# Kernel tuning notes

Measured on AMD Instinct MI355X. Metric: run time of the kernel, lower is better.

Reference implementation:

```python
import jax, jax.numpy as jnp
import numpy as np

DOWN_RATIO = 4.0
K_DET = 300          # max detections kept per image (YOLOv5 default)
P_PTS = 128          # contour points per instance (deep-snake)
CONF_THR = 0.2
IOU_THR = 0.3
MAX_WH = 4096.0      # class offset for class-aware NMS
DILATIONS = (1, 1, 1, 2, 2, 4, 4)
N_ITER = 2           # snake evolution iterations


def cir_conv(x, w, b, dil):
    # circular 1D conv along point dim; x [N,C,P], w [O,C,K]
    k = w.shape[-1]
    pad = dil * (k - 1) // 2
    xp = jnp.concatenate([x[..., x.shape[-1] - pad:], x, x[..., :pad]], axis=-1)
    y = jax.lax.conv_general_dilated(xp, w, window_strides=(1,), padding='VALID',
                                     rhs_dilation=(dil,),
                                     dimension_numbers=('NCH', 'OIH', 'NCH'))
    return y + b[None, :, None]


def snake_offsets(z, w_head, b_head, w_res, b_res, w_fuse, b_fuse, w_p1, b_p1, w_p2, b_p2):
    # z [N,66,P] -> offsets [N,2,P]
    states = [z]
    x = jax.nn.relu(cir_conv(z, w_head, b_head, 1))
    states.append(x)
    for i, d in enumerate(DILATIONS):
        x = jax.nn.relu(cir_conv(x, w_res[i], b_res[i], d)) + x
        states.append(x)
    state = jnp.concatenate(states, axis=1)            # [N,1090,P]
    fused = jax.nn.relu(cir_conv(state, w_fuse, b_fuse, 1))  # [N,256,P]
    h = jax.nn.relu(cir_conv(fused, w_p1, b_p1, 1))
    return cir_conv(h, w_p2, b_p2, 1)                  # [N,2,P]


def bilinear_sample(feat, pts):
    # feat [C,H,W]; pts [K,P,2] (x,y) in feature pixels -> [K,C,P]
    C, H, W = feat.shape
    x = jnp.clip(pts[..., 0], 0.0, W - 1.0)
    y = jnp.clip(pts[..., 1], 0.0, H - 1.0)
    x0f = jnp.clip(jnp.floor(x), 0.0, W - 2.0)
    y0f = jnp.clip(jnp.floor(y), 0.0, H - 2.0)
    x0 = x0f.astype(jnp.int32); y0 = y0f.astype(jnp.int32)
    dx = x - x0f; dy = y - y0f
    f = feat.reshape(C, H * W)
    def g(ix, iy):
        return f[:, iy * W + ix]                       # [C,K,P]
    out = (g(x0, y0) * (1 - dx) * (1 - dy) + g(x0 + 1, y0) * dx * (1 - dy)
           + g(x0, y0 + 1) * (1 - dx) * dy + g(x0 + 1, y0 + 1) * dx * dy)
    return out.transpose(1, 0, 2)


def nms_single(boxes, scores, cls):
    # boxes [K,4] xyxy sorted desc by score; class-aware greedy NMS -> keep mask [K]
    K = boxes.shape[0]
    b = boxes + cls[:, None] * MAX_WH
    area = (b[:, 2] - b[:, 0]) * (b[:, 3] - b[:, 1])
    lt = jnp.maximum(b[:, None, :2], b[None, :, :2])
    rb = jnp.minimum(b[:, None, 2:], b[None, :, 2:])
    wh = jnp.clip(rb - lt, 0.0)
    inter = wh[..., 0] * wh[..., 1]
    iou = inter / (area[:, None] + area[None, :] - inter + 1e-9)
    def body(i, keep):
        sup = (iou[i] > IOU_THR) & (jnp.arange(K) > i) & keep[i]
        return keep & (~sup)
    return jax.lax.fori_loop(0, K, body, jnp.ones((K,), bool))


def reference(pred, feat, conv_w, conv_b, w_head, b_head, w_res, b_res,
              w_fuse, b_fuse, w_p1, b_p1, w_p2, b_p2):
    B, N, D = pred.shape
    # ---- non_max_suppression(pred, 0.2, 0.3) ----
    score_all = pred[..., 4:5] * pred[..., 5:]          # obj * cls
    score = score_all.max(-1)                           # [B,N]
    cls = jnp.argmax(score_all, -1)                     # [B,N]
    s_masked = jnp.where(score > CONF_THR, score, 0.0)
    top_s, top_i = jax.lax.top_k(s_masked, K_DET)       # [B,K]
    xywh = jnp.take_along_axis(pred[..., :4], top_i[..., None], axis=1)
    boxes = jnp.concatenate([xywh[..., :2] - xywh[..., 2:] / 2,
                             xywh[..., :2] + xywh[..., 2:] / 2], axis=-1)
    cls_k = jnp.take_along_axis(cls, top_i, axis=1).astype(jnp.float32)
    keep = jax.vmap(nms_single)(boxes, top_s, cls_k)
    valid = keep & (top_s > CONF_THR)                   # [B,K]
    detection = jnp.concatenate([boxes, top_s[..., None], cls_k[..., None]], -1)
    boxes_ds = boxes / DOWN_RATIO                       # feature-scale boxes
    ct = jnp.stack([(boxes_ds[..., 0] + boxes_ds[..., 2]) / 2,
                    (boxes_ds[..., 1] + boxes_ds[..., 3]) / 2], -1)  # [B,K,2]
    Bf, C, H, W = feat.shape
    up = jax.image.resize(feat, (Bf, C, 2 * H, 2 * W), method='linear')
    cf = jax.lax.conv_general_dilated(up, conv_w, (1, 1), 'SAME',
                                      dimension_numbers=('NCHW', 'OIHW', 'NCHW'))
    cf = jax.nn.silu(cf + conv_b[None, :, None, None])  # [B,64,160,160]
    # ---- snake contour evolution ----
    half = jnp.maximum((boxes_ds[..., 2:] - boxes_ds[..., :2]) / 2, 1e-3)  # [B,K,2]
    theta = jnp.arange(P_PTS, dtype=jnp.float32) * (2 * np.pi / P_PTS)
    ring = jnp.stack([jnp.cos(theta), jnp.sin(theta)], -1)                 # [P,2]
    pts = ct[:, :, None, :] + half[:, :, None, :] * ring[None, None]       # [B,K,P,2]
    for _ in range(N_ITER):
        fpts = jax.vmap(bilinear_sample)(cf, pts)                          # [B,K,64,P]
        rel = ((pts - ct[:, :, None, :]) / half[:, :, None, :]).transpose(0, 1, 3, 2)
        z = jnp.concatenate([fpts, rel], axis=2)                           # [B,K,66,P]
        z = z.reshape(B * K_DET, 66, P_PTS)
        off = snake_offsets(z, w_head, b_head, w_res, b_res, w_fuse, b_fuse,
                            w_p1, b_p1, w_p2, b_p2)
        pts = pts + off.reshape(B, K_DET, 2, P_PTS).transpose(0, 1, 3, 2)
    pts = pts * valid[..., None, None].astype(pts.dtype)
    return detection, ct, pts, valid


def setup_inputs():
    key = jax.random.key(0)
    ks = jax.random.split(key, 16)
    B, N, NC = 16, 25200, 80
    cx = jax.random.uniform(ks[0], (B, N, 1)) * 640.0
    cy = jax.random.uniform(ks[1], (B, N, 1)) * 640.0
    w = jax.random.uniform(ks[2], (B, N, 1)) * 120.0 + 8.0
    h = jax.random.uniform(ks[3], (B, N, 1)) * 120.0 + 8.0
    conf = jax.random.uniform(ks[4], (B, N, 1 + NC))
    pred = jnp.concatenate([cx, cy, w, h, conf], -1)
    feat = jax.random.normal(ks[5], (B, 128, 80, 80))
    p = lambda k, s: jax.random.normal(k, s) * 0.05
    return {
        'pred': pred, 'feat': feat,
        'conv_w': p(ks[6], (64, 128, 3, 3)), 'conv_b': jnp.zeros((64,)),
        'w_head': p(ks[7], (128, 66, 9)), 'b_head': jnp.zeros((128,)),
        'w_res': p(ks[8], (7, 128, 128, 9)), 'b_res': jnp.zeros((7, 128)),
        'w_fuse': p(ks[9], (256, 1090, 1)), 'b_fuse': jnp.zeros((256,)),
        'w_p1': p(ks[10], (64, 256, 1)), 'b_p1': jnp.zeros((64,)),
        'w_p2': p(ks[11], (2, 64, 1)), 'b_p2': jnp.zeros((2,)),
    }
```

## Files before the change

kernel.cpp:

```cpp
#include <hip/hip_runtime.h>
#include <hip/hip_bf16.h>
#include <math.h>

typedef unsigned int u32;
typedef unsigned long long u64;
typedef unsigned short u16;

#define NB 16
#define NPRED 25200
#define ND 85
#define NCLS 80
#define KDET 300
#define PPTS 128
#define NINST (NB*KDET)
#define CONF_T 0.2f
#define IOU_T 0.3f
#define MAX_WH_ 4096.0f
#define NBKT 8192

#define CH 1120
#define STROW 143360

typedef __attribute__((ext_vector_type(8))) short bhalf8;
typedef __attribute__((ext_vector_type(4))) float f32x4;

__device__ __forceinline__ float b2f(u16 u){ return __uint_as_float((u32)u << 16); }
__device__ __forceinline__ u16 f2b(float v){ __hip_bfloat16 h = __float2bfloat16(v); return *(u16*)&h; }

__global__ __launch_bounds__(256) void k_score(const float* __restrict__ pred,
        float* __restrict__ score, int* __restrict__ cls){
  int i = blockIdx.x*256 + threadIdx.x;
  if (i >= NB*NPRED) return;
  const float* r = pred + (size_t)i*ND;
  float obj = r[4];
  float best = obj*r[5]; int bc = 0;
  for (int c = 1; c < NCLS; ++c){
    float v = obj*r[5+c];
    if (v > best){ best = v; bc = c; }
  }
  score[i] = (best > CONF_T) ? best : 0.f;
  cls[i] = bc;
}

__global__ __launch_bounds__(1024) void k_topk(const float* __restrict__ score,
        int* __restrict__ top_i, float* __restrict__ top_s){
  __shared__ int hist[NBKT];
  __shared__ int part[1024];
  __shared__ u64 keys[1024];
  __shared__ int s_bstar, s_cnt;
  int b = blockIdx.x, t = threadIdx.x;
  const float* s = score + (size_t)b*NPRED;
  for (int i = t; i < NBKT; i += 1024) hist[i] = 0;
  __syncthreads();
  for (int i = t; i < NPRED; i += 1024){
    float v = s[i];
    if (v > 0.f){
      int bk = (int)(v * (float)NBKT); if (bk > NBKT-1) bk = NBKT-1;
      atomicAdd(&hist[bk], 1);
    }
  }
  __syncthreads();
  int psum = 0;
  for (int j = 0; j < 8; ++j) psum += hist[t*8+j];
  part[t] = psum;
  __syncthreads();
  if (t == 0){
    int cum = 0, bstar = 0;
    for (int q = 1023; q >= 0; --q){
      if (cum + part[q] >= KDET){
        int c2 = cum; int bb;
        for (bb = q*8+7; bb >= q*8; --bb){
          c2 += hist[bb];
          if (c2 >= KDET) break;
        }
        if (bb < q*8) bb = q*8;
        bstar = bb;
        break;
      }
      cum += part[q];
    }
    s_bstar = bstar;
    s_cnt = 0;
  }
  keys[t] = 0ull;
  __syncthreads();
  int bstar = s_bstar;
  for (int i = t; i < NPRED; i += 1024){
    float v = s[i];
    if (v > 0.f){
      int bk = (int)(v * (float)NBKT); if (bk > NBKT-1) bk = NBKT-1;
      if (bk >= bstar){
        int pos = atomicAdd(&s_cnt, 1);
        if (pos < 1024){
          keys[pos] = ((u64)__float_as_uint(v) << 32) | (u32)(~(u32)i);
        }
      }
    }
  }
  __syncthreads();
  for (int k = 2; k <= 1024; k <<= 1){
    for (int j = k>>1; j > 0; j >>= 1){
      int ixj = t ^ j;
      if (ixj > t){
        u64 a = keys[t], c = keys[ixj];
        bool up = ((t & k) == 0);
        bool sw = up ? (a < c) : (a > c);
        if (sw){ keys[t] = c; keys[ixj] = a; }
      }
      __syncthreads();
    }
  }
  if (t < KDET){
    u64 key = keys[t];
    float v; int idx;
    if (key == 0ull){ v = 0.f; idx = 0; }
    else { v = __uint_as_float((u32)(key >> 32)); idx = (int)(~(u32)(key & 0xffffffffull)); }
    top_s[b*KDET + t] = v;
    top_i[b*KDET + t] = idx;
  }
}

__global__ __launch_bounds__(384) void k_nms(const float* __restrict__ pred,
        const int* __restrict__ top_i, const float* __restrict__ top_s,
        const int* __restrict__ clsb,
        float* __restrict__ det_out, float* __restrict__ ct_out, float* __restrict__ pts_out,
        float* __restrict__ ct_ws, float* __restrict__ half_ws, int* __restrict__ valid_ws){
  __shared__ float bx0[KDET], bx1[KDET], bx2[KDET], bx3[KDET], ar[KDET];
  __shared__ float rx0[KDET], rx1[KDET], rx2[KDET], rx3[KDET];
  __shared__ float sc[KDET], cl[KDET];
  __shared__ float ctxs[KDET], ctys[KDET], hxs[KDET], hys[KDET];
  __shared__ int keep[KDET];
  int b = blockIdx.x, t = threadIdx.x;
  for (int i = t; i < KDET; i += 384){
    int idx = top_i[b*KDET + i];
    const float* r = pred + ((size_t)b*NPRED + idx)*ND;
    float cx = r[0], cy = r[1], w = r[2], h = r[3];
    float x1 = cx - w/2.f, y1 = cy - h/2.f, x2 = cx + w/2.f, y2 = cy + h/2.f;
    float c = (float)clsb[(size_t)b*NPRED + idx];
    float o = c * MAX_WH_;
    float a0 = x1 + o, a1 = y1 + o, a2 = x2 + o, a3 = y2 + o;
    bx0[i]=a0; bx1[i]=a1; bx2[i]=a2; bx3[i]=a3;
    ar[i] = (a2-a0)*(a3-a1);
    rx0[i]=x1; rx1[i]=y1; rx2[i]=x2; rx3[i]=y2;
    sc[i] = top_s[b*KDET + i];
    cl[i] = c;
    keep[i] = 1;
  }
  __syncthreads();
  for (int i = 0; i < KDET; ++i){
    if (keep[i]){
      float b0=bx0[i], b1=bx1[i], b2=bx2[i], b3=bx3[i], ai=ar[i];
      for (int j = i+1+t; j < KDET; j += 384){
        float ltx = fmaxf(b0, bx0[j]);
        float lty = fmaxf(b1, bx1[j]);
        float rbx = fminf(b2, bx2[j]);
        float rby = fminf(b3, bx3[j]);
        float ww = rbx - ltx; ww = ww > 0.f ? ww : 0.f;
        float hh = rby - lty; hh = hh > 0.f ? hh : 0.f;
        float inter = ww*hh;
        float iou = inter / (ai + ar[j] - inter + 1e-9f);
        if (iou > IOU_T) keep[j] = 0;
      }
    }
    __syncthreads();
  }
  for (int i = t; i < KDET; i += 384){
    int v = (keep[i] && (sc[i] > CONF_T)) ? 1 : 0;
    valid_ws[b*KDET + i] = v;
    size_t o6 = ((size_t)b*KDET + i)*6;
    det_out[o6+0]=rx0[i]; det_out[o6+1]=rx1[i]; det_out[o6+2]=rx2[i]; det_out[o6+3]=rx3[i];
    det_out[o6+4]=sc[i];  det_out[o6+5]=cl[i];
    float bd0 = rx0[i]/4.f, bd1 = rx1[i]/4.f, bd2 = rx2[i]/4.f, bd3 = rx3[i]/4.f;
    float cx = (bd0+bd2)/2.f, cy = (bd1+bd3)/2.f;
    float hx = (bd2-bd0)/2.f; hx = hx > 1e-3f ? hx : 1e-3f;
    float hy = (bd3-bd1)/2.f; hy = hy > 1e-3f ? hy : 1e-3f;
    ct_out[((size_t)b*KDET+i)*2+0] = cx;
    ct_out[((size_t)b*KDET+i)*2+1] = cy;
    ct_ws[((size_t)b*KDET+i)*2+0] = cx;
    ct_ws[((size_t)b*KDET+i)*2+1] = cy;
    half_ws[((size_t)b*KDET+i)*2+0] = hx;
    half_ws[((size_t)b*KDET+i)*2+1] = hy;
    ctxs[i]=cx; ctys[i]=cy; hxs[i]=hx; hys[i]=hy;
  }
  __syncthreads();
  for (int e = t; e < KDET*PPTS; e += 384){
    int i = e >> 7, p = e & 127;
    float th = (float)p * 0.04908738521234052f;
    size_t o = ((size_t)(b*KDET + i)*PPTS + p)*2;
    pts_out[o+0] = ctxs[i] + hxs[i]*cosf(th);
    pts_out[o+1] = ctys[i] + hys[i]*sinf(th);
  }
}

__global__ __launch_bounds__(256) void k_cnn(const float* __restrict__ feat,
        const float* __restrict__ cw, const float* __restrict__ cb,
        __hip_bfloat16* __restrict__ cf){
  __shared__ float up[324];
  __shared__ float wl[576];
  int b = blockIdx.x;
  int tile = blockIdx.y;
  int ty0 = (tile/10)*16, tx0 = (tile - (tile/10)*10)*16;
  int t = threadIdx.x;
  int py = t >> 4, px = t & 15;
  int oy = ty0 + py, ox = tx0 + px;
  float acc[64];
  #pragma unroll
  for (int o = 0; o < 64; ++o) acc[o] = 0.f;
  for (int ic = 0; ic < 128; ++ic){
    __syncthreads();
    const float* fin = feat + ((size_t)b*128 + ic)*6400;
    for (int u = t; u < 324; u += 256){
      int r = u/18;
      int uy = ty0 - 1 + r, ux = tx0 - 1 + (u - r*18);
      float val = 0.f;
      if (uy >= 0 && uy < 160 && ux >= 0 && ux < 160){
        float cyf = 0.5f*(float)uy - 0.25f;
        float cxf = 0.5f*(float)ux - 0.25f;
        float fy0 = floorf(cyf), fx0 = floorf(cxf);
        float fy = cyf - fy0, fx = cxf - fx0;
        int y0 = (int)fy0, x0 = (int)fx0;
        int y0c = y0 < 0 ? 0 : (y0 > 79 ? 79 : y0);
        int y1c = y0+1 > 79 ? 79 : (y0+1 < 0 ? 0 : y0+1);
        int x0c = x0 < 0 ? 0 : (x0 > 79 ? 79 : x0);
        int x1c = x0+1 > 79 ? 79 : (x0+1 < 0 ? 0 : x0+1);
        float v00 = fin[y0c*80+x0c], v01 = fin[y0c*80+x1c];
        float v10 = fin[y1c*80+x0c], v11 = fin[y1c*80+x1c];
        val = v00*(1.f-fy)*(1.f-fx) + v01*(1.f-fy)*fx + v10*fy*(1.f-fx) + v11*fy*fx;
      }
      up[u] = val;
    }
    for (int u = t; u < 576; u += 256){
      int o = u/9;
      wl[u] = cw[((size_t)o*128 + ic)*9 + (u - o*9)];
    }
    __syncthreads();
    float v[9];
    #pragma unroll
    for (int k = 0; k < 9; ++k)
      v[k] = up[(py + k/3)*18 + (px + k%3)];
    #pragma unroll
    for (int o = 0; o < 64; ++o){
      float a = acc[o];
      #pragma unroll
      for (int k = 0; k < 9; ++k) a += wl[o*9+k]*v[k];
      acc[o] = a;
    }
  }
  size_t base = ((size_t)b*64)*25600 + (size_t)oy*160 + ox;
  #pragma unroll
  for (int o = 0; o < 64; ++o){
    float x = acc[o] + cb[o];
    float sg = 1.f / (1.f + __expf(-x));
    cf[base + (size_t)o*25600] = __float2bfloat16(x*sg);
  }
}

__global__ __launch_bounds__(256) void k_sample(const __hip_bfloat16* __restrict__ cf,
        const float* __restrict__ pts, const float* __restrict__ ct_ws,
        const float* __restrict__ half_ws, __hip_bfloat16* __restrict__ states,
        int base, int cnt){
  int e = blockIdx.x*256 + threadIdx.x;
  if (e >= cnt*PPTS) return;
  int li = e >> 7, p = e & 127;
  int g = base + li;
  int b = g / KDET;
  size_t po = ((size_t)g*PPTS + p)*2;
  float px = pts[po], py = pts[po+1];
  float ctx = ct_ws[g*2], cty = ct_ws[g*2+1];
  float hx = half_ws[g*2], hy = half_ws[g*2+1];
  __align__(16) u16 zl[66];
  zl[64] = f2b((px - ctx)/hx);
  zl[65] = f2b((py - cty)/hy);
  float x = px < 0.f ? 0.f : (px > 159.f ? 159.f : px);
  float y = py < 0.f ? 0.f : (py > 159.f ? 159.f : py);
  float x0f = floorf(x); x0f = x0f < 0.f ? 0.f : (x0f > 158.f ? 158.f : x0f);
  float y0f = floorf(y); y0f = y0f < 0.f ? 0.f : (y0f > 158.f ? 158.f : y0f);
  float dx = x - x0f, dy = y - y0f;
  int x0 = (int)x0f, y0 = (int)y0f;
  float w00 = (1.f-dx)*(1.f-dy), w01 = dx*(1.f-dy), w10 = (1.f-dx)*dy, w11 = dx*dy;
  const __hip_bfloat16* f = cf + (size_t)b*64*25600 + (size_t)y0*160 + x0;
  for (int c = 0; c < 64; ++c){
    const __hip_bfloat16* fc = f + (size_t)c*25600;
    float v00 = __bfloat162float(fc[0]);
    float v01 = __bfloat162float(fc[1]);
    float v10 = __bfloat162float(fc[160]);
    float v11 = __bfloat162float(fc[161]);
    zl[c] = f2b(v00*w00 + v01*w01 + v10*w10 + v11*w11);
  }
  u16* dst = (u16*)states + ((size_t)li*128 + p)*CH + 1024;
  #pragma unroll
  for (int w2 = 0; w2 < 64; w2 += 8) *(uint4*)(dst + w2) = *(const uint4*)(zl + w2);
  *(u32*)(dst + 64) = *(const u32*)(zl + 64);
}


template<int NSUB>
__device__ __forceinline__ void g_load_a(bhalf8* dst, const u16* Xb, int s, int dil,
                                         int rg0, int r16, int hi){
  int k = s / NSUB;
  int icb = (s - k*NSUB)*64 + hi*16;
  int shift = (k - 4)*dil;
  #pragma unroll
  for (int g = 0; g < 4; ++g){
    int row = (rg0 + g*16 + r16 + shift + 128) & 127;
    dst[g] = *(const bhalf8*)((const char*)Xb + row*256 + (icb ^ ((row & 7) << 4)));
  }
}
__device__ __forceinline__ void g_load_b(bhalf8* dst, const bhalf8* wf, int s, int lane, int sstride){
  const bhalf8* w = wf + (size_t)s*sstride + lane;
  #pragma unroll
  for (int ct = 0; ct < 8; ++ct) dst[ct] = w[ct*64];
}

#define MFMA_SET(A_, B_) { \
  _Pragma("unroll") \
  for (int g_ = 0; g_ < 4; ++g_){ \
    _Pragma("unroll") \
    for (int ct_ = 0; ct_ < 8; ++ct_) \
      acc[g_][ct_] = __builtin_amdgcn_mfma_f32_16x16x32_bf16((A_)[g_], (B_)[ct_], acc[g_][ct_], 0, 0, 0); \
  } }

template<int NSUB>
__device__ __forceinline__ void gemm_run(const u16* Xb, const bhalf8* wf, int s0, int s1,
    int dil, int rg0, int r16, int hi, int lane, f32x4 acc[4][8], int sstride){
  bhalf8 aA[4], bA[8], aB[4], bB[8];
  g_load_a<NSUB>(aA, Xb, s0, dil, rg0, r16, hi);
  g_load_b(bA, wf, s0, lane, sstride);
  int s = s0;
  for (; s + 1 < s1; s += 2){
    g_load_a<NSUB>(aB, Xb, s+1, dil, rg0, r16, hi);
    g_load_b(bB, wf, s+1, lane, sstride);
    MFMA_SET(aA, bA);
    if (s + 2 < s1){
      g_load_a<NSUB>(aA, Xb, s+2, dil, rg0, r16, hi);
      g_load_b(bA, wf, s+2, lane, sstride);
    }
    MFMA_SET(aB, bB);
  }
  if (s < s1) MFMA_SET(aA, bA);
}

__device__ __forceinline__ void epilogue(f32x4 acc[4][8], u16* Y, const u16* Xc,
    const float* __restrict__ bias, u16* gout, int gstride, int rg0, int r16, int hi){
  #pragma unroll
  for (int g = 0; g < 4; ++g){
    #pragma unroll
    for (int ct = 0; ct < 8; ++ct){
      int oc = ct*16 + r16;
      float bv = bias[oc];
      #pragma unroll
      for (int rr = 0; rr < 4; ++rr){
        int p = rg0 + g*16 + hi*4 + rr;
        float v = acc[g][ct][rr] + bv;
        v = v > 0.f ? v : 0.f;
        int lidx = (p*256 + ((oc*2) ^ ((p & 7) << 4))) >> 1;
        if (Xc) v += b2f(Xc[lidx]);
        u16 hu = f2b(v);
        if (Y) Y[lidx] = hu;
        gout[(size_t)p*gstride + oc] = hu;
      }
    }
  }
}

__global__ __launch_bounds__(128) void k_mega(__hip_bfloat16* __restrict__ states_,
    const u16* __restrict__ wfh, const float* __restrict__ bh,
    const u16* __restrict__ wfr, const float* __restrict__ brs){
  __shared__ u16 X[2][16384];
  int t = threadIdx.x, lane = t & 63, wid = t >> 6;
  int r16 = lane & 15, hi = lane >> 4;
  int rg0 = wid*64;
  u16* st = (u16*)states_ + (size_t)blockIdx.x*STROW;
  const bhalf8* WH = (const bhalf8*)wfh;
  const bhalf8* WR = (const bhalf8*)wfr;
  f32x4 acc[4][8];

  for (int i = t; i < 2048; i += 128){
    int p = i >> 4, c = i & 15;
    if (c < 12){
      uint4 v = *(const uint4*)(st + (size_t)p*CH + 1024 + c*8);
      *(uint4*)((char*)X[0] + p*256 + ((c*16) ^ ((p & 7) << 4))) = v;
    }
  }
  __syncthreads();

  #pragma unroll
  for (int g = 0; g < 4; ++g)
    #pragma unroll
    for (int ct = 0; ct < 8; ++ct) acc[g][ct] = (f32x4){0.f,0.f,0.f,0.f};
  gemm_run<3>(X[0], WH, 0, 27, 1, rg0, r16, hi, lane, acc, 512);
  epilogue(acc, X[1], nullptr, bh, st, CH, rg0, r16, hi);
  __syncthreads();

  int cur = 1;
  #pragma unroll 1
  for (int l = 0; l < 7; ++l){
    int dil = (l < 3) ? 1 : ((l < 5) ? 2 : 4);
    #pragma unroll
    for (int g = 0; g < 4; ++g)
      #pragma unroll
      for (int ct = 0; ct < 8; ++ct) acc[g][ct] = (f32x4){0.f,0.f,0.f,0.f};
    gemm_run<4>(X[cur], WR + (size_t)l*18432, 0, 36, dil, rg0, r16, hi, lane, acc, 512);
    epilogue(acc, X[cur^1], X[cur], brs + l*128, st + 128*(l+1), CH, rg0, r16, hi);
    __syncthreads();
    cur ^= 1;
  }
}

__global__ __launch_bounds__(256) void k_fuse(const __hip_bfloat16* __restrict__ states_,
    __hip_bfloat16* __restrict__ fusedb, const u16* __restrict__ wff,
    const float* __restrict__ bfu){
  __shared__ u16 XF[2][16384];
  int t = threadIdx.x, lane = t & 63, wid = t >> 6;
  int r16 = lane & 15, hi = lane >> 4;
  int wr = wid & 1, wc = wid >> 1;
  int rg0 = wr*64;
  const u16* st = (const u16*)states_ + (size_t)blockIdx.x*STROW;
  const bhalf8* WFp = (const bhalf8*)wff + wc*512;
  f32x4 acc[4][8];
  #pragma unroll
  for (int g = 0; g < 4; ++g)
    #pragma unroll
    for (int ct = 0; ct < 8; ++ct) acc[g][ct] = (f32x4){0.f,0.f,0.f,0.f};
  #pragma unroll 1
  for (int cc = 0; cc < 9; ++cc){
    __syncthreads();
    int ch0 = cc*128, nc = (cc == 8) ? 12 : 16;
    for (int i = t; i < 2048; i += 256){
      int p = i >> 4, c = i & 15;
      if (c < nc){
        uint4 v = *(const uint4*)(st + (size_t)p*CH + ch0 + c*8);
        *(uint4*)((char*)XF[cc & 1] + p*256 + ((c*16) ^ ((p & 7) << 4))) = v;
      }
    }
    __syncthreads();
    int s0 = cc*4, s1 = (cc == 8) ? 35 : (s0 + 4);
    gemm_run<4>(XF[cc & 1], WFp, s0, s1, 0, rg0, r16, hi, lane, acc, 1024);
  }
  u16* fo = (u16*)fusedb + (size_t)blockIdx.x*32768 + wc*128;
  epilogue(acc, nullptr, nullptr, bfu + wc*128, fo, 256, rg0, r16, hi);
}

__global__ __launch_bounds__(128) void k_p1p2(const __hip_bfloat16* __restrict__ fusedbuf,
        const float* __restrict__ wp1r, const float* __restrict__ bp1,
        const float* __restrict__ wp2, const float* __restrict__ bp2,
        float* __restrict__ pts, int base){
  int inst = blockIdx.x, p = threadIdx.x;
  const u16* f = (const u16*)fusedbuf + (size_t)inst*32768 + (size_t)p*256;
  float h[64];
  #pragma unroll
  for (int o = 0; o < 64; ++o) h[o] = bp1[o];
  for (int c8 = 0; c8 < 32; ++c8){
    uint4 v = *(const uint4*)(f + c8*8);
    const u16* vv = (const u16*)&v;
    #pragma unroll
    for (int j = 0; j < 8; ++j){
      float x = b2f(vv[j]);
      const float* w = wp1r + (size_t)(c8*8 + j)*64;
      #pragma unroll
      for (int o = 0; o < 64; ++o) h[o] += w[o]*x;
    }
  }
  float ox = bp2[0], oy = bp2[1];
  #pragma unroll
  for (int o = 0; o < 64; ++o){
    float hv = h[o] > 0.f ? h[o] : 0.f;
    ox += wp2[o]*hv;
    oy += wp2[64+o]*hv;
  }
  int g = base + inst;
  size_t po = ((size_t)g*PPTS + p)*2;
  pts[po]   += ox;
  pts[po+1] += oy;
}

__global__ __launch_bounds__(256) void k_final(float* __restrict__ pts,
        const int* __restrict__ valid_ws, float* __restrict__ valid_out){
  int e = blockIdx.x*256 + threadIdx.x;
  if (e < NINST) valid_out[e] = valid_ws[e] ? 1.f : 0.f;
  if (e < NINST*PPTS){
    float m = valid_ws[e >> 7] ? 1.f : 0.f;
    pts[(size_t)e*2]   *= m;
    pts[(size_t)e*2+1] *= m;
  }
}

__global__ __launch_bounds__(256) void k_pack_head(const float* __restrict__ w, u16* __restrict__ out){
  int e = blockIdx.x*256 + threadIdx.x;
  if (e >= 110592) return;
  int j = e & 7, l = (e >> 3) & 63, ct = (e >> 9) & 7, s = e >> 12;
  int oc = ct*16 + (l & 15);
  int k = s/3, icq = s - k*3;
  int ic = icq*32 + (l >> 4)*8 + j;
  float v = (ic < 66) ? w[(oc*66 + ic)*9 + k] : 0.f;
  out[e] = f2b(v);
}
__global__ __launch_bounds__(256) void k_pack_res(const float* __restrict__ w, u16* __restrict__ out){
  int e = blockIdx.x*256 + threadIdx.x;
  if (e >= 1032192) return;
  int lay = e / 147456, r = e - lay*147456;
  int j = r & 7, l = (r >> 3) & 63, ct = (r >> 9) & 7, s = r >> 12;
  int oc = ct*16 + (l & 15);
  int k = s >> 2;
  int ic = (s & 3)*32 + (l >> 4)*8 + j;
  out[e] = f2b(w[((size_t)(lay*128 + oc)*128 + ic)*9 + k]);
}
__global__ __launch_bounds__(256) void k_pack_fuse(const float* __restrict__ w, u16* __restrict__ out){
  int e = blockIdx.x*256 + threadIdx.x;
  if (e >= 286720) return;
  int j = e & 7, l = (e >> 3) & 63, ct = (e >> 9) & 15, s = e >> 13;
  int oc = ct*16 + (l & 15);
  int ch = s*32 + (l >> 4)*8 + j;
  float v = 0.f;
  if (ch < 1024) v = w[(size_t)oc*1090 + 66 + ch];
  else if (ch < 1090) v = w[(size_t)oc*1090 + (ch - 1024)];
  out[e] = f2b(v);
}
__global__ __launch_bounds__(256) void k_repack_p1(const float* __restrict__ w, float* __restrict__ wr){
  int e = blockIdx.x*256 + threadIdx.x;
  if (e >= 64*256) return;
  int oc = e / 256, ic = e - oc*256;
  wr[ic*64 + oc] = w[e];
}

extern "C" void kernel_launch(void* const* d_in, const int* in_sizes, int n_in,
                              void* d_out, int out_size, void* d_ws, size_t ws_size,
                              hipStream_t stream){
  (void)in_sizes; (void)n_in; (void)out_size;
  const float* pred   = (const float*)d_in[0];
  const float* feat   = (const float*)d_in[1];
  const float* conv_w = (const float*)d_in[2];
  const float* conv_b = (const float*)d_in[3];
  const float* w_head = (const float*)d_in[4];
  const float* b_head = (const float*)d_in[5];
  const float* w_res  = (const float*)d_in[6];
  const float* b_res  = (const float*)d_in[7];
  const float* w_fuse = (const float*)d_in[8];
  const float* b_fuse = (const float*)d_in[9];
  const float* w_p1   = (const float*)d_in[10];
  const float* b_p1   = (const float*)d_in[11];
  const float* w_p2   = (const float*)d_in[12];
  const float* b_p2   = (const float*)d_in[13];

  float* out = (float*)d_out;
  float* det_out   = out;
  float* ct_out    = out + 28800;
  float* pts_out   = out + 38400;
  float* valid_out = out + 1267200;

  char* wsb = (char*)d_ws;
  size_t woff = 0;
  auto walloc = [&](size_t bytes)->char*{
    char* p = wsb + woff;
    woff += (bytes + 255) & ~(size_t)255;
    return p;
  };
  __hip_bfloat16* cf = (__hip_bfloat16*)walloc((size_t)16*64*160*160*2);
  float* score   = (float*)walloc((size_t)NB*NPRED*4);
  int*   clsb    = (int*)  walloc((size_t)NB*NPRED*4);
  int*   top_i   = (int*)  walloc((size_t)NINST*4);
  float* top_s   = (float*)walloc((size_t)NINST*4);
  float* ct_ws   = (float*)walloc((size_t)NINST*2*4);
  float* half_ws = (float*)walloc((size_t)NINST*2*4);
  int*   valid_ws= (int*)  walloc((size_t)NINST*4);
  u16*   wfh     = (u16*)  walloc((size_t)110592*2);
  u16*   wfr     = (u16*)  walloc((size_t)1032192*2);
  u16*   wff     = (u16*)  walloc((size_t)286720*2);
  float* wr_p1   = (float*)walloc((size_t)16384*4);

  size_t per_inst = (size_t)STROW*2 + (size_t)32768*2;
  long long avail = (long long)ws_size - (long long)woff;
  int C = (int)(avail / (long long)per_inst);
  if (C > NINST) C = NINST;
  if (C < 1) C = 1;
  __hip_bfloat16* states   = (__hip_bfloat16*)walloc((size_t)C*STROW*2);
  __hip_bfloat16* fusedbuf = (__hip_bfloat16*)walloc((size_t)C*32768*2);

  k_pack_head<<<(110592+255)/256, 256, 0, stream>>>(w_head, wfh);
  k_pack_res <<<(1032192+255)/256, 256, 0, stream>>>(w_res, wfr);
  k_pack_fuse<<<(286720+255)/256, 256, 0, stream>>>(w_fuse, wff);
  k_repack_p1<<<(16384+255)/256, 256, 0, stream>>>(w_p1, wr_p1);

  k_score<<<(NB*NPRED+255)/256, 256, 0, stream>>>(pred, score, clsb);
  k_topk <<<NB, 1024, 0, stream>>>(score, top_i, top_s);
  k_nms  <<<NB, 384, 0, stream>>>(pred, top_i, top_s, clsb, det_out, ct_out, pts_out,
                                  ct_ws, half_ws, valid_ws);
  k_cnn  <<<dim3(16,100), 256, 0, stream>>>(feat, conv_w, conv_b, cf);

  for (int it = 0; it < 2; ++it){
    for (int base = 0; base < NINST; base += C){
      int cnt = NINST - base; if (cnt > C) cnt = C;
      k_sample<<<(cnt*PPTS+255)/256, 256, 0, stream>>>(cf, pts_out, ct_ws, half_ws, states, base, cnt);
      k_mega<<<cnt, 128, 0, stream>>>(states, wfh, b_head, wfr, b_res);
      k_fuse<<<cnt, 256, 0, stream>>>(states, fusedbuf, wff, b_fuse);
      k_p1p2<<<cnt, 128, 0, stream>>>(fusedbuf, wr_p1, b_p1, w_p2, b_p2, pts_out, base);
    }
  }
  k_final<<<(NINST*PPTS+255)/256, 256, 0, stream>>>(pts_out, valid_ws, valid_out);
}
```

Before: 10.87 ms.

## Fuse snake pipeline into one persistent kernel and retile the upsample conv

Sampling, head and residual convs, fuse conv, p1 and p2 now run in a single persistent kernel. Each block loops over instances for both snake iterations, replacing the per-chunk sequence of four launches and the intermediate fused buffer round-trip through global memory. The p1 layer moves from scalar FP32 to bf16 MFMA using a new packed weight layout. The CNN kernel is retiled to 8x8 tiles with output-channel groups across waves, processing two input channels per step and reading weights straight from global memory. The risk is lower occupancy and longer-lived blocks with more syncs, plus bf16 rounding in p1.

```diff
diff --git a/kernel.cpp b/kernel.cpp
--- a/kernel.cpp
+++ b/kernel.cpp
@@ -26,6 +26,7 @@
 
 __device__ __forceinline__ float b2f(u16 u){ return __uint_as_float((u32)u << 16); }
 __device__ __forceinline__ u16 f2b(float v){ __hip_bfloat16 h = __float2bfloat16(v); return *(u16*)&h; }
+#define SWZ(p) (((p)&7)<<4)
 
 __global__ __launch_bounds__(256) void k_score(const float* __restrict__ pred,
         float* __restrict__ score, int* __restrict__ cls){
@@ -195,25 +196,25 @@
 __global__ __launch_bounds__(256) void k_cnn(const float* __restrict__ feat,
         const float* __restrict__ cw, const float* __restrict__ cb,
         __hip_bfloat16* __restrict__ cf){
-  __shared__ float up[324];
-  __shared__ float wl[576];
-  int b = blockIdx.x;
-  int tile = blockIdx.y;
-  int ty0 = (tile/10)*16, tx0 = (tile - (tile/10)*10)*16;
+  __shared__ float up[2][120];
+  int b = blockIdx.x, tile = blockIdx.y;
+  int ty0 = (tile/20)*8, tx0 = (tile - (tile/20)*20)*8;
   int t = threadIdx.x;
-  int py = t >> 4, px = t & 15;
-  int oy = ty0 + py, ox = tx0 + px;
-  float acc[64];
+  int og = t >> 6, lane = t & 63;
+  int py = lane >> 3, px = lane & 7;
+  float acc[16];
   #pragma unroll
-  for (int o = 0; o < 64; ++o) acc[o] = 0.f;
-  for (int ic = 0; ic < 128; ++ic){
+  for (int oo = 0; oo < 16; ++oo) acc[oo] = 0.f;
+  #pragma unroll 1
+  for (int ic = 0; ic < 128; ic += 2){
     __syncthreads();
-    const float* fin = feat + ((size_t)b*128 + ic)*6400;
-    for (int u = t; u < 324; u += 256){
-      int r = u/18;
-      int uy = ty0 - 1 + r, ux = tx0 - 1 + (u - r*18);
+    if (t < 200){
+      int which = t/100, u = t - which*100;
+      int r = u/10, cix = u - r*10;
+      int uy = ty0 - 1 + r, ux = tx0 - 1 + cix;
       float val = 0.f;
       if (uy >= 0 && uy < 160 && ux >= 0 && ux < 160){
+        const float* fin = feat + ((size_t)b*128 + ic + which)*6400;
         float cyf = 0.5f*(float)uy - 0.25f;
         float cxf = 0.5f*(float)ux - 0.25f;
         float fy0 = floorf(cyf), fx0 = floorf(cxf);
@@ -227,72 +228,34 @@
         float v10 = fin[y1c*80+x0c], v11 = fin[y1c*80+x1c];
         val = v00*(1.f-fy)*(1.f-fx) + v01*(1.f-fy)*fx + v10*fy*(1.f-fx) + v11*fy*fx;
       }
-      up[u] = val;
-    }
-    for (int u = t; u < 576; u += 256){
-      int o = u/9;
-      wl[u] = cw[((size_t)o*128 + ic)*9 + (u - o*9)];
+      up[which][r*12 + cix] = val;
     }
     __syncthreads();
-    float v[9];
     #pragma unroll
-    for (int k = 0; k < 9; ++k)
-      v[k] = up[(py + k/3)*18 + (px + k%3)];
-    #pragma unroll
-    for (int o = 0; o < 64; ++o){
-      float a = acc[o];
+    for (int which = 0; which < 2; ++which){
+      float v[9];
       #pragma unroll
-      for (int k = 0; k < 9; ++k) a += wl[o*9+k]*v[k];
-      acc[o] = a;
-    }
-  }
-  size_t base = ((size_t)b*64)*25600 + (size_t)oy*160 + ox;
+      for (int k = 0; k < 9; ++k)
+        v[k] = up[which][(py + k/3)*12 + (px + k%3)];
+      #pragma unroll
+      for (int oo = 0; oo < 16; ++oo){
+        const float* w9 = cw + ((size_t)(og*16 + oo)*128 + ic + which)*9;
+        float a = acc[oo];
+        #pragma unroll
+        for (int k = 0; k < 9; ++k) a += w9[k]*v[k];
+        acc[oo] = a;
+      }
+    }
+  }
+  int oy = ty0 + py, ox = tx0 + px;
   #pragma unroll
-  for (int o = 0; o < 64; ++o){
-    float x = acc[o] + cb[o];
+  for (int oo = 0; oo < 16; ++oo){
+    int oc = og*16 + oo;
+    float x = acc[oo] + cb[oc];
     float sg = 1.f / (1.f + __expf(-x));
-    cf[base + (size_t)o*25600] = __float2bfloat16(x*sg);
-  }
-}
-
-__global__ __launch_bounds__(256) void k_sample(const __hip_bfloat16* __restrict__ cf,
-        const float* __restrict__ pts, const float* __restrict__ ct_ws,
-        const float* __restrict__ half_ws, __hip_bfloat16* __restrict__ states,
-        int base, int cnt){
-  int e = blockIdx.x*256 + threadIdx.x;
-  if (e >= cnt*PPTS) return;
-  int li = e >> 7, p = e & 127;
-  int g = base + li;
-  int b = g / KDET;
-  size_t po = ((size_t)g*PPTS + p)*2;
-  float px = pts[po], py = pts[po+1];
-  float ctx = ct_ws[g*2], cty = ct_ws[g*2+1];
-  float hx = half_ws[g*2], hy = half_ws[g*2+1];
-  __align__(16) u16 zl[66];
-  zl[64] = f2b((px - ctx)/hx);
-  zl[65] = f2b((py - cty)/hy);
-  float x = px < 0.f ? 0.f : (px > 159.f ? 159.f : px);
-  float y = py < 0.f ? 0.f : (py > 159.f ? 159.f : py);
-  float x0f = floorf(x); x0f = x0f < 0.f ? 0.f : (x0f > 158.f ? 158.f : x0f);
-  float y0f = floorf(y); y0f = y0f < 0.f ? 0.f : (y0f > 158.f ? 158.f : y0f);
-  float dx = x - x0f, dy = y - y0f;
-  int x0 = (int)x0f, y0 = (int)y0f;
-  float w00 = (1.f-dx)*(1.f-dy), w01 = dx*(1.f-dy), w10 = (1.f-dx)*dy, w11 = dx*dy;
-  const __hip_bfloat16* f = cf + (size_t)b*64*25600 + (size_t)y0*160 + x0;
-  for (int c = 0; c < 64; ++c){
-    const __hip_bfloat16* fc = f + (size_t)c*25600;
-    float v00 = __bfloat162float(fc[0]);
-    float v01 = __bfloat162float(fc[1]);
-    float v10 = __bfloat162float(fc[160]);
-    float v11 = __bfloat162float(fc[161]);
-    zl[c] = f2b(v00*w00 + v01*w01 + v10*w10 + v11*w11);
-  }
-  u16* dst = (u16*)states + ((size_t)li*128 + p)*CH + 1024;
-  #pragma unroll
-  for (int w2 = 0; w2 < 64; w2 += 8) *(uint4*)(dst + w2) = *(const uint4*)(zl + w2);
-  *(u32*)(dst + 64) = *(const u32*)(zl + 64);
-}
-
+    cf[((size_t)b*64 + oc)*25600 + (size_t)oy*160 + ox] = __float2bfloat16(x*sg);
+  }
+}
 
 template<int NSUB>
 __device__ __forceinline__ void g_load_a(bhalf8* dst, const u16* Xb, int s, int dil,
@@ -303,175 +266,275 @@
   #pragma unroll
   for (int g = 0; g < 4; ++g){
     int row = (rg0 + g*16 + r16 + shift + 128) & 127;
-    dst[g] = *(const bhalf8*)((const char*)Xb + row*256 + (icb ^ ((row & 7) << 4)));
-  }
-}
-__device__ __forceinline__ void g_load_b(bhalf8* dst, const bhalf8* wf, int s, int lane, int sstride){
-  const bhalf8* w = wf + (size_t)s*sstride + lane;
+    dst[g] = *(const bhalf8*)((const char*)Xb + row*256 + (icb ^ SWZ(row)));
+  }
+}
+template<int NCT>
+__device__ __forceinline__ void g_load_b(bhalf8* dst, const bhalf8* wf, int s, int ctbase,
+                                         int lane, int sstride){
+  const bhalf8* w = wf + (size_t)s*sstride + ctbase*64 + lane;
   #pragma unroll
-  for (int ct = 0; ct < 8; ++ct) dst[ct] = w[ct*64];
-}
-
-#define MFMA_SET(A_, B_) { \
-  _Pragma("unroll") \
-  for (int g_ = 0; g_ < 4; ++g_){ \
-    _Pragma("unroll") \
-    for (int ct_ = 0; ct_ < 8; ++ct_) \
-      acc[g_][ct_] = __builtin_amdgcn_mfma_f32_16x16x32_bf16((A_)[g_], (B_)[ct_], acc[g_][ct_], 0, 0, 0); \
-  } }
-
-template<int NSUB>
+  for (int ct = 0; ct < NCT; ++ct) dst[ct] = w[ct*64];
+}
+
+template<int NSUB, int NCT, bool DBUF>
 __device__ __forceinline__ void gemm_run(const u16* Xb, const bhalf8* wf, int s0, int s1,
-    int dil, int rg0, int r16, int hi, int lane, f32x4 acc[4][8], int sstride){
-  bhalf8 aA[4], bA[8], aB[4], bB[8];
-  g_load_a<NSUB>(aA, Xb, s0, dil, rg0, r16, hi);
-  g_load_b(bA, wf, s0, lane, sstride);
-  int s = s0;
-  for (; s + 1 < s1; s += 2){
-    g_load_a<NSUB>(aB, Xb, s+1, dil, rg0, r16, hi);
-    g_load_b(bB, wf, s+1, lane, sstride);
-    MFMA_SET(aA, bA);
-    if (s + 2 < s1){
-      g_load_a<NSUB>(aA, Xb, s+2, dil, rg0, r16, hi);
-      g_load_b(bA, wf, s+2, lane, sstride);
-    }
-    MFMA_SET(aB, bB);
-  }
-  if (s < s1) MFMA_SET(aA, bA);
-}
-
-__device__ __forceinline__ void epilogue(f32x4 acc[4][8], u16* Y, const u16* Xc,
-    const float* __restrict__ bias, u16* gout, int gstride, int rg0, int r16, int hi){
-  #pragma unroll
-  for (int g = 0; g < 4; ++g){
-    #pragma unroll
-    for (int ct = 0; ct < 8; ++ct){
-      int oc = ct*16 + r16;
-      float bv = bias[oc];
+    int dil, int rg0, int ctbase, int r16, int hi, int lane, f32x4 (&acc)[4][NCT], int sstride){
+  if (DBUF){
+    bhalf8 aA[4], bA[NCT], aB[4], bB[NCT];
+    g_load_a<NSUB>(aA, Xb, s0, dil, rg0, r16, hi);
+    g_load_b<NCT>(bA, wf, s0, ctbase, lane, sstride);
+    int s = s0;
+    for (; s + 1 < s1; s += 2){
+      g_load_a<NSUB>(aB, Xb, s+1, dil, rg0, r16, hi);
+      g_load_b<NCT>(bB, wf, s+1, ctbase, lane, sstride);
       #pragma unroll
-      for (int rr = 0; rr < 4; ++rr){
-        int p = rg0 + g*16 + hi*4 + rr;
-        float v = acc[g][ct][rr] + bv;
-        v = v > 0.f ? v : 0.f;
-        int lidx = (p*256 + ((oc*2) ^ ((p & 7) << 4))) >> 1;
-        if (Xc) v += b2f(Xc[lidx]);
-        u16 hu = f2b(v);
-        if (Y) Y[lidx] = hu;
-        gout[(size_t)p*gstride + oc] = hu;
-      }
-    }
-  }
-}
-
-__global__ __launch_bounds__(128) void k_mega(__hip_bfloat16* __restrict__ states_,
+      for (int g = 0; g < 4; ++g)
+        #pragma unroll
+        for (int ct = 0; ct < NCT; ++ct)
+          acc[g][ct] = __builtin_amdgcn_mfma_f32_16x16x32_bf16(aA[g], bA[ct], acc[g][ct], 0, 0, 0);
+      if (s + 2 < s1){
+        g_load_a<NSUB>(aA, Xb, s+2, dil, rg0, r16, hi);
+        g_load_b<NCT>(bA, wf, s+2, ctbase, lane, sstride);
+      }
+      #pragma unroll
+      for (int g = 0; g < 4; ++g)
+        #pragma unroll
+        for (int ct = 0; ct < NCT; ++ct)
+          acc[g][ct] = __builtin_amdgcn_mfma_f32_16x16x32_bf16(aB[g], bB[ct], acc[g][ct], 0, 0, 0);
+    }
+    if (s < s1){
+      #pragma unroll
+      for (int g = 0; g < 4; ++g)
+        #pragma unroll
+        for (int ct = 0; ct < NCT; ++ct)
+          acc[g][ct] = __builtin_amdgcn_mfma_f32_16x16x32_bf16(aA[g], bA[ct], acc[g][ct], 0, 0, 0);
+    }
+  } else {
+    for (int s = s0; s < s1; ++s){
+      bhalf8 a[4], bb[NCT];
+      g_load_a<NSUB>(a, Xb, s, dil, rg0, r16, hi);
+      g_load_b<NCT>(bb, wf, s, ctbase, lane, sstride);
+      #pragma unroll
+      for (int g = 0; g < 4; ++g)
+        #pragma unroll
+        for (int ct = 0; ct < NCT; ++ct)
+          acc[g][ct] = __builtin_amdgcn_mfma_f32_16x16x32_bf16(a[g], bb[ct], acc[g][ct], 0, 0, 0);
+    }
+  }
+}
+
+__global__ __launch_bounds__(256, 2) void k_snake(const __hip_bfloat16* __restrict__ cf_,
+    float* __restrict__ pts, const float* __restrict__ ct_ws, const float* __restrict__ half_ws,
+    u16* __restrict__ slabg,
     const u16* __restrict__ wfh, const float* __restrict__ bh,
-    const u16* __restrict__ wfr, const float* __restrict__ brs){
+    const u16* __restrict__ wfr, const float* __restrict__ brs,
+    const u16* __restrict__ wff, const float* __restrict__ bfu,
+    const u16* __restrict__ wp1f, const float* __restrict__ bp1,
+    const float* __restrict__ wp2, const float* __restrict__ bp2){
   __shared__ u16 X[2][16384];
-  int t = threadIdx.x, lane = t & 63, wid = t >> 6;
-  int r16 = lane & 15, hi = lane >> 4;
-  int rg0 = wid*64;
-  u16* st = (u16*)states_ + (size_t)blockIdx.x*STROW;
-  const bhalf8* WH = (const bhalf8*)wfh;
-  const bhalf8* WR = (const bhalf8*)wfr;
-  f32x4 acc[4][8];
-
-  for (int i = t; i < 2048; i += 128){
-    int p = i >> 4, c = i & 15;
-    if (c < 12){
-      uint4 v = *(const uint4*)(st + (size_t)p*CH + 1024 + c*8);
-      *(uint4*)((char*)X[0] + p*256 + ((c*16) ^ ((p & 7) << 4))) = v;
-    }
-  }
-  __syncthreads();
-
-  #pragma unroll
-  for (int g = 0; g < 4; ++g)
-    #pragma unroll
-    for (int ct = 0; ct < 8; ++ct) acc[g][ct] = (f32x4){0.f,0.f,0.f,0.f};
-  gemm_run<3>(X[0], WH, 0, 27, 1, rg0, r16, hi, lane, acc, 512);
-  epilogue(acc, X[1], nullptr, bh, st, CH, rg0, r16, hi);
-  __syncthreads();
-
-  int cur = 1;
-  #pragma unroll 1
-  for (int l = 0; l < 7; ++l){
-    int dil = (l < 3) ? 1 : ((l < 5) ? 2 : 4);
-    #pragma unroll
-    for (int g = 0; g < 4; ++g)
-      #pragma unroll
-      for (int ct = 0; ct < 8; ++ct) acc[g][ct] = (f32x4){0.f,0.f,0.f,0.f};
-    gemm_run<4>(X[cur], WR + (size_t)l*18432, 0, 36, dil, rg0, r16, hi, lane, acc, 512);
-    epilogue(acc, X[cur^1], X[cur], brs + l*128, st + 128*(l+1), CH, rg0, r16, hi);
-    __syncthreads();
-    cur ^= 1;
-  }
-}
-
-__global__ __launch_bounds__(256) void k_fuse(const __hip_bfloat16* __restrict__ states_,
-    __hip_bfloat16* __restrict__ fusedb, const u16* __restrict__ wff,
-    const float* __restrict__ bfu){
-  __shared__ u16 XF[2][16384];
+  __shared__ float pxy[128][2];
   int t = threadIdx.x, lane = t & 63, wid = t >> 6;
   int r16 = lane & 15, hi = lane >> 4;
   int wr = wid & 1, wc = wid >> 1;
-  int rg0 = wr*64;
-  const u16* st = (const u16*)states_ + (size_t)blockIdx.x*STROW;
-  const bhalf8* WFp = (const bhalf8*)wff + wc*512;
-  f32x4 acc[4][8];
-  #pragma unroll
-  for (int g = 0; g < 4; ++g)
-    #pragma unroll
-    for (int ct = 0; ct < 8; ++ct) acc[g][ct] = (f32x4){0.f,0.f,0.f,0.f};
+  int rgM = wr*64;
+  u16* slab = slabg + (size_t)blockIdx.x * STROW;
+  const bhalf8* WH = (const bhalf8*)wfh;
+  const bhalf8* WR = (const bhalf8*)wfr;
+  const bhalf8* WF = (const bhalf8*)wff;
+  const bhalf8* WP = (const bhalf8*)wp1f;
+  const u16* cfu = (const u16*)cf_;
+
   #pragma unroll 1
-  for (int cc = 0; cc < 9; ++cc){
-    __syncthreads();
-    int ch0 = cc*128, nc = (cc == 8) ? 12 : 16;
-    for (int i = t; i < 2048; i += 256){
-      int p = i >> 4, c = i & 15;
-      if (c < nc){
-        uint4 v = *(const uint4*)(st + (size_t)p*CH + ch0 + c*8);
-        *(uint4*)((char*)XF[cc & 1] + p*256 + ((c*16) ^ ((p & 7) << 4))) = v;
-      }
-    }
-    __syncthreads();
-    int s0 = cc*4, s1 = (cc == 8) ? 35 : (s0 + 4);
-    gemm_run<4>(XF[cc & 1], WFp, s0, s1, 0, rg0, r16, hi, lane, acc, 1024);
-  }
-  u16* fo = (u16*)fusedb + (size_t)blockIdx.x*32768 + wc*128;
-  epilogue(acc, nullptr, nullptr, bfu + wc*128, fo, 256, rg0, r16, hi);
-}
-
-__global__ __launch_bounds__(128) void k_p1p2(const __hip_bfloat16* __restrict__ fusedbuf,
-        const float* __restrict__ wp1r, const float* __restrict__ bp1,
-        const float* __restrict__ wp2, const float* __restrict__ bp2,
-        float* __restrict__ pts, int base){
-  int inst = blockIdx.x, p = threadIdx.x;
-  const u16* f = (const u16*)fusedbuf + (size_t)inst*32768 + (size_t)p*256;
-  float h[64];
-  #pragma unroll
-  for (int o = 0; o < 64; ++o) h[o] = bp1[o];
-  for (int c8 = 0; c8 < 32; ++c8){
-    uint4 v = *(const uint4*)(f + c8*8);
-    const u16* vv = (const u16*)&v;
-    #pragma unroll
-    for (int j = 0; j < 8; ++j){
-      float x = b2f(vv[j]);
-      const float* w = wp1r + (size_t)(c8*8 + j)*64;
-      #pragma unroll
-      for (int o = 0; o < 64; ++o) h[o] += w[o]*x;
-    }
-  }
-  float ox = bp2[0], oy = bp2[1];
-  #pragma unroll
-  for (int o = 0; o < 64; ++o){
-    float hv = h[o] > 0.f ? h[o] : 0.f;
-    ox += wp2[o]*hv;
-    oy += wp2[64+o]*hv;
-  }
-  int g = base + inst;
-  size_t po = ((size_t)g*PPTS + p)*2;
-  pts[po]   += ox;
-  pts[po+1] += oy;
+  for (int inst = blockIdx.x; inst < NINST; inst += gridDim.x){
+    if (t < 128){
+      pxy[t][0] = pts[(size_t)inst*256 + t*2];
+      pxy[t][1] = pts[(size_t)inst*256 + t*2 + 1];
+    }
+    float ctx = ct_ws[inst*2], cty = ct_ws[inst*2+1];
+    float hx = half_ws[inst*2], hy = half_ws[inst*2+1];
+    int bimg = inst / KDET;
+
+    #pragma unroll 1
+    for (int iter = 0; iter < 2; ++iter){
+      __syncthreads();
+      {
+        int p = t & 127, hf = t >> 7;
+        float px = pxy[p][0], py = pxy[p][1];
+        float x = px < 0.f ? 0.f : (px > 159.f ? 159.f : px);
+        float y = py < 0.f ? 0.f : (py > 159.f ? 159.f : py);
+        float x0f = floorf(x); x0f = x0f < 0.f ? 0.f : (x0f > 158.f ? 158.f : x0f);
+        float y0f = floorf(y); y0f = y0f < 0.f ? 0.f : (y0f > 158.f ? 158.f : y0f);
+        float dx = x - x0f, dy = y - y0f;
+        int x0 = (int)x0f, y0 = (int)y0f;
+        float w00 = (1.f-dx)*(1.f-dy), w01 = dx*(1.f-dy), w10 = (1.f-dx)*dy, w11 = dx*dy;
+        const u16* f = cfu + (size_t)bimg*64*25600 + (size_t)y0*160 + x0;
+        __align__(16) u16 zl[32];
+        for (int c = 0; c < 32; ++c){
+          const u16* fc = f + (size_t)(hf*32 + c)*25600;
+          float v00 = b2f(fc[0]), v01 = b2f(fc[1]);
+          float v10 = b2f(fc[160]), v11 = b2f(fc[161]);
+          zl[c] = f2b(v00*w00 + v01*w01 + v10*w10 + v11*w11);
+        }
+        char* xrow = (char*)X[0] + p*256;
+        u16* zs = slab + (size_t)p*CH + 1024 + hf*32;
+        #pragma unroll
+        for (int q = 0; q < 4; ++q){
+          *(uint4*)(xrow + ((hf*64 + q*16) ^ SWZ(p))) = ((const uint4*)zl)[q];
+          *(uint4*)(zs + q*8) = ((const uint4*)zl)[q];
+        }
+        uint4 z4; z4.x = 0; z4.y = 0; z4.z = 0; z4.w = 0;
+        if (hf == 0){
+          __align__(16) u16 ex[8];
+          ex[0] = f2b((px - ctx)/hx); ex[1] = f2b((py - cty)/hy);
+          #pragma unroll
+          for (int j = 2; j < 8; ++j) ex[j] = 0;
+          *(uint4*)(xrow + (128 ^ SWZ(p))) = *(const uint4*)ex;
+          *(uint4*)(slab + (size_t)p*CH + 1088) = *(const uint4*)ex;
+        } else {
+          *(uint4*)(xrow + (144 ^ SWZ(p))) = z4;
+          *(uint4*)(xrow + (160 ^ SWZ(p))) = z4;
+          *(uint4*)(xrow + (176 ^ SWZ(p))) = z4;
+          *(uint4*)(slab + (size_t)p*CH + 1096) = z4;
+          *(uint4*)(slab + (size_t)p*CH + 1104) = z4;
+          *(uint4*)(slab + (size_t)p*CH + 1112) = z4;
+        }
+      }
+      __syncthreads();
+      int cur = 0;
+      #pragma unroll 1
+      for (int l = -1; l < 7; ++l){
+        f32x4 acc[4][4];
+        #pragma unroll
+        for (int g = 0; g < 4; ++g)
+          #pragma unroll
+          for (int ct = 0; ct < 4; ++ct) acc[g][ct] = (f32x4){0.f,0.f,0.f,0.f};
+        const float* bias;
+        u16* slout;
+        if (l < 0){
+          gemm_run<3,4,true>(X[0], WH, 0, 27, 1, rgM, wc*4, r16, hi, lane, acc, 512);
+          bias = bh; slout = slab;
+        } else {
+          int dil = (l < 3) ? 1 : ((l < 5) ? 2 : 4);
+          gemm_run<4,4,true>(X[cur], WR + (size_t)l*18432, 0, 36, dil, rgM, wc*4, r16, hi, lane, acc, 512);
+          bias = brs + l*128; slout = slab + 128*(l+1);
+        }
+        u16* Y = X[cur^1];
+        const u16* Xc = (l < 0) ? nullptr : X[cur];
+        #pragma unroll
+        for (int g = 0; g < 4; ++g){
+          #pragma unroll
+          for (int ct = 0; ct < 4; ++ct){
+            int oc = (wc*4 + ct)*16 + r16;
+            float bv = bias[oc];
+            #pragma unroll
+            for (int rr = 0; rr < 4; ++rr){
+              int p = rgM + g*16 + hi*4 + rr;
+              float v = acc[g][ct][rr] + bv;
+              v = v > 0.f ? v : 0.f;
+              int lidx = (p*256 + ((oc*2) ^ SWZ(p))) >> 1;
+              if (Xc) v += b2f(Xc[lidx]);
+              u16 hu = f2b(v);
+              Y[lidx] = hu;
+              slout[(size_t)p*CH + oc] = hu;
+            }
+          }
+        }
+        __syncthreads();
+        cur ^= 1;
+      }
+      {
+        f32x4 acc[4][8];
+        #pragma unroll
+        for (int g = 0; g < 4; ++g)
+          #pragma unroll
+          for (int ct = 0; ct < 8; ++ct) acc[g][ct] = (f32x4){0.f,0.f,0.f,0.f};
+        #pragma unroll 1
+        for (int cc = 0; cc < 9; ++cc){
+          __syncthreads();
+          int ch0 = cc*128, nc = (cc == 8) ? 12 : 16;
+          for (int i = t; i < 2048; i += 256){
+            int p = i >> 4, c = i & 15;
+            if (c < nc){
+              uint4 v = *(const uint4*)(slab + (size_t)p*CH + ch0 + c*8);
+              *(uint4*)((char*)X[cc & 1] + p*256 + ((c*16) ^ SWZ(p))) = v;
+            }
+          }
+          __syncthreads();
+          int s0 = cc*4, s1 = (cc == 8) ? 35 : (s0 + 4);
+          gemm_run<4,8,false>(X[cc & 1], WF, s0, s1, 0, rgM, wc*8, r16, hi, lane, acc, 1024);
+        }
+        __syncthreads();
+        #pragma unroll
+        for (int g = 0; g < 4; ++g){
+          #pragma unroll
+          for (int ct = 0; ct < 8; ++ct){
+            int ocg = (wc*8 + ct)*16 + r16;
+            float bv = bfu[ocg];
+            u16* Yb = X[ocg >> 7];
+            int col = ocg & 127;
+            #pragma unroll
+            for (int rr = 0; rr < 4; ++rr){
+              int p = rgM + g*16 + hi*4 + rr;
+              float v = acc[g][ct][rr] + bv;
+              v = v > 0.f ? v : 0.f;
+              Yb[(p*256 + ((col*2) ^ SWZ(p))) >> 1] = f2b(v);
+            }
+          }
+        }
+      }
+      __syncthreads();
+      {
+        f32x4 acc[4][2];
+        #pragma unroll
+        for (int g = 0; g < 4; ++g)
+          #pragma unroll
+          for (int ct = 0; ct < 2; ++ct) acc[g][ct] = (f32x4){0.f,0.f,0.f,0.f};
+        gemm_run<4,2,true>(X[0], WP, 0, 4, 0, rgM, wc*2, r16, hi, lane, acc, 256);
+        gemm_run<4,2,true>(X[1], WP, 4, 8, 0, rgM, wc*2, r16, hi, lane, acc, 256);
+        __syncthreads();
+        #pragma unroll
+        for (int g = 0; g < 4; ++g){
+          #pragma unroll
+          for (int ct = 0; ct < 2; ++ct){
+            int oc = (wc*2 + ct)*16 + r16;
+            float bv = bp1[oc];
+            #pragma unroll
+            for (int rr = 0; rr < 4; ++rr){
+              int p = rgM + g*16 + hi*4 + rr;
+              float v = acc[g][ct][rr] + bv;
+              v = v > 0.f ? v : 0.f;
+              X[0][(p*256 + ((oc*2) ^ SWZ(p))) >> 1] = f2b(v);
+            }
+          }
+        }
+      }
+      __syncthreads();
+      if (t < 128){
+        int p = t;
+        float ox = bp2[0], oy = bp2[1];
+        #pragma unroll
+        for (int j8 = 0; j8 < 8; ++j8){
+          uint4 u = *(const uint4*)((const char*)X[0] + p*256 + ((j8*16) ^ SWZ(p)));
+          __align__(16) u16 hh[8];
+          *(uint4*)hh = u;
+          #pragma unroll
+          for (int j = 0; j < 8; ++j){
+            float hv = b2f(hh[j]);
+            int oc = j8*8 + j;
+            ox += wp2[oc]*hv;
+            oy += wp2[64 + oc]*hv;
+          }
+        }
+        pxy[p][0] += ox;
+        pxy[p][1] += oy;
+      }
+    }
+    if (t < 128){
+      pts[(size_t)inst*256 + t*2]     = pxy[t][0];
+      pts[(size_t)inst*256 + t*2 + 1] = pxy[t][1];
+    }
+  }
 }
 
 __global__ __launch_bounds__(256) void k_final(float* __restrict__ pts,
@@ -516,11 +579,13 @@
   else if (ch < 1090) v = w[(size_t)oc*1090 + (ch - 1024)];
   out[e] = f2b(v);
 }
-__global__ __launch_bounds__(256) void k_repack_p1(const float* __restrict__ w, float* __restrict__ wr){
+__global__ __launch_bounds__(256) void k_pack_p1(const float* __restrict__ w, u16* __restrict__ out){
   int e = blockIdx.x*256 + threadIdx.x;
-  if (e >= 64*256) return;
-  int oc = e / 256, ic = e - oc*256;
-  wr[ic*64 + oc] = w[e];
+  if (e >= 16384) return;
+  int j = e & 7, l = (e >> 3) & 63, ct = (e >> 9) & 3, s = e >> 11;
+  int oc = ct*16 + (l & 15);
+  int ic = s*32 + (l >> 4)*8 + j;
+  out[e] = f2b(w[oc*256 + ic]);
 }
 
 extern "C" void kernel_launch(void* const* d_in, const int* in_sizes, int n_in,
@@ -566,35 +631,29 @@
   u16*   wfh     = (u16*)  walloc((size_t)110592*2);
   u16*   wfr     = (u16*)  walloc((size_t)1032192*2);
   u16*   wff     = (u16*)  walloc((size_t)286720*2);
-  float* wr_p1   = (float*)walloc((size_t)16384*4);
-
-  size_t per_inst = (size_t)STROW*2 + (size_t)32768*2;
+  u16*   wp1f    = (u16*)  walloc((size_t)16384*2);
+
   long long avail = (long long)ws_size - (long long)woff;
-  int C = (int)(avail / (long long)per_inst);
-  if (C > NINST) C = NINST;
-  if (C < 1) C = 1;
-  __hip_bfloat16* states   = (__hip_bfloat16*)walloc((size_t)C*STROW*2);
-  __hip_bfloat16* fusedbuf = (__hip_bfloat16*)walloc((size_t)C*32768*2);
+  int G = (int)(avail / (long long)(STROW*2));
+  if (G > 1024) G = 1024;
+  if (G > NINST) G = NINST;
+  if (G < 1) G = 1;
+  u16* slabg = (u16*)walloc((size_t)G*STROW*2);
 
   k_pack_head<<<(110592+255)/256, 256, 0, stream>>>(w_head, wfh);
   k_pack_res <<<(1032192+255)/256, 256, 0, stream>>>(w_res, wfr);
   k_pack_fuse<<<(286720+255)/256, 256, 0, stream>>>(w_fuse, wff);
-  k_repack_p1<<<(16384+255)/256, 256, 0, stream>>>(w_p1, wr_p1);
+  k_pack_p1  <<<(16384+255)/256, 256, 0, stream>>>(w_p1, wp1f);
 
   k_score<<<(NB*NPRED+255)/256, 256, 0, stream>>>(pred, score, clsb);
   k_topk <<<NB, 1024, 0, stream>>>(score, top_i, top_s);
   k_nms  <<<NB, 384, 0, stream>>>(pred, top_i, top_s, clsb, det_out, ct_out, pts_out,
                                   ct_ws, half_ws, valid_ws);
-  k_cnn  <<<dim3(16,100), 256, 0, stream>>>(feat, conv_w, conv_b, cf);
-
-  for (int it = 0; it < 2; ++it){
-    for (int base = 0; base < NINST; base += C){
-      int cnt = NINST - base; if (cnt > C) cnt = C;
-      k_sample<<<(cnt*PPTS+255)/256, 256, 0, stream>>>(cf, pts_out, ct_ws, half_ws, states, base, cnt);
-      k_mega<<<cnt, 128, 0, stream>>>(states, wfh, b_head, wfr, b_res);
-      k_fuse<<<cnt, 256, 0, stream>>>(states, fusedbuf, wff, b_fuse);
-      k_p1p2<<<cnt, 128, 0, stream>>>(fusedbuf, wr_p1, b_p1, w_p2, b_p2, pts_out, base);
-    }
-  }
+  k_cnn  <<<dim3(16,400), 256, 0, stream>>>(feat, conv_w, conv_b, cf);
+
+  k_snake<<<G, 256, 0, stream>>>(cf, pts_out, ct_ws, half_ws, slabg,
+                                 wfh, b_head, wfr, b_res, wff, b_fuse,
+                                 wp1f, b_p1, w_p2, b_p2);
+
   k_final<<<(NINST*PPTS+255)/256, 256, 0, stream>>>(pts_out, valid_ws, valid_out);
 }
```

Result: faster. 10.15 ms (-6.6%).
